# Kernel tuning notes

Measured on AMD Instinct MI355X. Metric: run time of the kernel, lower is better.

## Reference

```python
import jax, jax.numpy as jnp
import numpy as np

V_TH = 0.4
V_RESET = 0.0
REFRAC = 3.0
ALPHA = 5.0

# Heaviside spike with surrogate-gradient (fast-sigmoid) backward, matching SpikeFnSTE.
@jax.custom_vjp
def spike(x):
    return (x > 0).astype(x.dtype)

def _spike_fwd(x):
    return spike(x), x

def _spike_bwd(x, g):
    return (g * (ALPHA / (1.0 + jnp.abs(ALPHA * x)) ** 2),)

spike.defvjp(_spike_fwd, _spike_bwd)


def setup_inputs() -> dict:
    key = jax.random.key(0)
    k1, k2 = jax.random.split(key)
    B, T, F, C = 128, 1000, 2048, 10
    x_seq = jax.random.bernoulli(k1, 0.05, (B, T, F)).astype(jnp.float32)
    # kaiming_normal_ on [F, C]: fan computed over in_features
    W = jax.random.normal(k2, (F, C), dtype=jnp.float32) * np.float32(np.sqrt(2.0 / F))
    return {"x_seq": x_seq, "W": W}


def reference(x_seq, W):
    B, T, F = x_seq.shape
    C = W.shape[1]

    def step(carry, x_t):
        V, refr, counts = carry
        I_t = x_t @ W                                  # [B, C]
        active = (refr <= 0).astype(V.dtype)
        V = V + I_t * active
        s = spike(V - V_TH) * active                   # [B, C] in {0,1}
        fired = s > 0
        V = jnp.where(fired, V_RESET, V)
        counts = counts + s
        refr = jnp.where(fired, REFRAC, refr)
        refr = jnp.maximum(refr - 1.0, 0.0)
        return (V, refr, counts), None

    init = (jnp.zeros((B, C), x_seq.dtype),
            jnp.zeros((B, C), x_seq.dtype),
            jnp.zeros((B, C), x_seq.dtype))
    # scan over time: x_seq [B,T,F] -> [T,B,F]
    (_, _, spike_counts), _ = jax.lax.scan(step, init, jnp.swapaxes(x_seq, 0, 1))
    return spike_counts
```

## Files before the change

### kernel.cpp

```cpp
#include <hip/hip_runtime.h>
#include <hip/hip_bf16.h>

#define T_TOTAL 1000
#define B_TOTAL 128
#define F_TOTAL 2048
#define C_OUT   10
#define NEUR    (B_TOTAL * C_OUT)

#define KSTEPS  (F_TOTAL / 32)
#define NBFRAG  (KSTEPS * 3 * 64)

typedef __attribute__((ext_vector_type(8))) short bf16x8;
typedef __attribute__((ext_vector_type(4))) float f32x4;

__global__ __launch_bounds__(256) void snn_prep(const float* __restrict__ W,
                                                uint4* __restrict__ bfrag)
{
    const int idx = blockIdx.x * 256 + threadIdx.x;
    if (idx >= NBFRAG) return;
    const int l = idx & 63;
    const int sp = idx >> 6;
    const int p = sp % 3;
    const int s = sp / 3;
    const int g = l >> 4, r = l & 15;
    unsigned out[4] = {0u, 0u, 0u, 0u};
#pragma unroll
    for (int j = 0; j < 8; ++j) {
        const int k = s * 32 + g * 8 + j;
        const float wv = (r < C_OUT) ? W[k * C_OUT + r] : 0.f;
        __hip_bfloat16 bh = __float2bfloat16(wv);
        const float fh = __bfloat162float(bh);
        __hip_bfloat16 bm = __float2bfloat16(wv - fh);
        const float fm = __bfloat162float(bm);
        __hip_bfloat16 bl = __float2bfloat16(wv - fh - fm);
        __hip_bfloat16 sel = (p == 0) ? bh : (p == 1) ? bm : bl;
        const unsigned short bits = *reinterpret_cast<unsigned short*>(&sel);
        out[j >> 1] |= (unsigned)bits << (16 * (j & 1));
    }
    bfrag[idx] = make_uint4(out[0], out[1], out[2], out[3]);
}

__global__ __launch_bounds__(256) void snn_phase1_mfma(
    const float* __restrict__ x, const uint4* __restrict__ bfrag,
    float* __restrict__ Ibuf, int t0, int cur)
{
    const int b  = blockIdx.y;
    const int w  = threadIdx.x >> 6;
    const int l  = threadIdx.x & 63;
    const int r  = l & 15, g = l >> 4;
    const int ttbase = blockIdx.x * 64 + w * 16;

    int t_row = t0 + ttbase + r;
    if (t_row > T_TOTAL - 1) t_row = T_TOTAL - 1;
    const float* __restrict__ arow =
        x + ((size_t)b * T_TOTAL + t_row) * F_TOTAL + g * 8;

    f32x4 acc = {0.f, 0.f, 0.f, 0.f};
    const uint4* __restrict__ bp = bfrag + l;

#pragma unroll 2
    for (int s = 0; s < KSTEPS; ++s) {
        const float4 a0 = *reinterpret_cast<const float4*>(arow + s * 32);
        const float4 a1 = *reinterpret_cast<const float4*>(arow + s * 32 + 4);
        const uint4 b0 = bp[(s * 3 + 0) * 64];
        const uint4 b1 = bp[(s * 3 + 1) * 64];
        const uint4 b2 = bp[(s * 3 + 2) * 64];
        union { bf16x8 v; unsigned u[4]; } af;
        af.u[0] = __builtin_amdgcn_perm(__float_as_uint(a0.y), __float_as_uint(a0.x), 0x07060302u);
        af.u[1] = __builtin_amdgcn_perm(__float_as_uint(a0.w), __float_as_uint(a0.z), 0x07060302u);
        af.u[2] = __builtin_amdgcn_perm(__float_as_uint(a1.y), __float_as_uint(a1.x), 0x07060302u);
        af.u[3] = __builtin_amdgcn_perm(__float_as_uint(a1.w), __float_as_uint(a1.z), 0x07060302u);
        union { bf16x8 v; uint4 q; } bb0, bb1, bb2;
        bb0.q = b0; bb1.q = b1; bb2.q = b2;
        acc = __builtin_amdgcn_mfma_f32_16x16x32_bf16(af.v, bb0.v, acc, 0, 0, 0);
        acc = __builtin_amdgcn_mfma_f32_16x16x32_bf16(af.v, bb1.v, acc, 0, 0, 0);
        acc = __builtin_amdgcn_mfma_f32_16x16x32_bf16(af.v, bb2.v, acc, 0, 0, 0);
    }

    const int tt4 = ttbase + 4 * g;
    if (r < C_OUT && tt4 + 3 < cur) {
        const float4 v = make_float4(acc[0], acc[1], acc[2], acc[3]);
        *reinterpret_cast<float4*>(&Ibuf[((size_t)b * C_OUT + r) * cur + tt4]) = v;
    }
}

__device__ __forceinline__ void snn_step(float Iv, float& V, float& refr, float& cnt)
{
    const bool act = (refr <= 0.f);
    V += act ? Iv : 0.f;
    const bool fired = act && ((V - 0.4f) > 0.f);
    cnt += fired ? 1.f : 0.f;
    V    = fired ? 0.f : V;
    refr = fired ? 3.f : refr;
    refr = fmaxf(refr - 1.f, 0.f);
}

__global__ __launch_bounds__(256) void snn_phase2(
    const float* __restrict__ Ibuf, float* __restrict__ state,
    float* __restrict__ out, int t0, int Tc, int last)
{
    const int n = blockIdx.x * 256 + threadIdx.x;
    if (n >= NEUR) return;

    float V, refr, cnt;
    if (t0 == 0) { V = 0.f; refr = 0.f; cnt = 0.f; }
    else { V = state[n]; refr = state[NEUR + n]; cnt = state[2 * NEUR + n]; }

    const float* __restrict__ I = Ibuf + (size_t)n * Tc;

    int i = 0;
    for (; i + 16 <= Tc; i += 16) {
        const float4 a = *reinterpret_cast<const float4*>(I + i);
        const float4 b = *reinterpret_cast<const float4*>(I + i + 4);
        const float4 c = *reinterpret_cast<const float4*>(I + i + 8);
        const float4 d = *reinterpret_cast<const float4*>(I + i + 12);
        snn_step(a.x, V, refr, cnt); snn_step(a.y, V, refr, cnt);
        snn_step(a.z, V, refr, cnt); snn_step(a.w, V, refr, cnt);
        snn_step(b.x, V, refr, cnt); snn_step(b.y, V, refr, cnt);
        snn_step(b.z, V, refr, cnt); snn_step(b.w, V, refr, cnt);
        snn_step(c.x, V, refr, cnt); snn_step(c.y, V, refr, cnt);
        snn_step(c.z, V, refr, cnt); snn_step(c.w, V, refr, cnt);
        snn_step(d.x, V, refr, cnt); snn_step(d.y, V, refr, cnt);
        snn_step(d.z, V, refr, cnt); snn_step(d.w, V, refr, cnt);
    }
    for (; i < Tc; ++i) snn_step(I[i], V, refr, cnt);

    if (last) {
        out[n] = cnt;
    } else {
        state[n] = V; state[NEUR + n] = refr; state[2 * NEUR + n] = cnt;
    }
}

extern "C" void kernel_launch(void* const* d_in, const int* in_sizes, int n_in,
                              void* d_out, int out_size, void* d_ws, size_t ws_size,
                              hipStream_t stream)
{
    const float* x = (const float*)d_in[0];
    const float* W = (const float*)d_in[1];
    float* out = (float*)d_out;

    float* state = (float*)d_ws;
    uint4* bfrag = (uint4*)((char*)d_ws + 3 * NEUR * sizeof(float));
    float* Ibuf  = (float*)((char*)d_ws + 3 * NEUR * sizeof(float) + NBFRAG * 16);

    snn_prep<<<(NBFRAG + 255) / 256, 256, 0, stream>>>(W, bfrag);

    const size_t head = 3 * NEUR + NBFRAG * 4;
    const size_t ws_floats = ws_size / sizeof(float);
    long avail = (long)ws_floats - (long)head;
    int Tc = (avail > 0) ? (int)(avail / NEUR) : 0;
    if (Tc > T_TOTAL) Tc = T_TOTAL;
    Tc &= ~3;
    if (Tc <= 0) Tc = 4;

    for (int t0 = 0; t0 < T_TOTAL; t0 += Tc) {
        int cur = T_TOTAL - t0; if (cur > Tc) cur = Tc;
        dim3 g1((cur + 63) / 64, B_TOTAL, 1);
        snn_phase1_mfma<<<g1, 256, 0, stream>>>(x, bfrag, Ibuf, t0, cur);
        const int last = (t0 + cur >= T_TOTAL) ? 1 : 0;
        snn_phase2<<<(NEUR + 255) / 256, 256, 0, stream>>>(Ibuf, state, out, t0, cur, last);
    }
}
```

Before: 310.9 us.

## Process two time-row tiles per wave and software-pipeline the K loop

Each wave now computes two 16-row M tiles, so every loaded B fragment (the three bf16 split weight pieces) feeds two MFMAs instead of one, halving B-fragment traffic per output. The K loop is manually double-buffered so the next step's loads are issued before the current step's MFMAs. The grid shrinks to half as many blocks along time. This raises register pressure and cuts parallelism, and the kernel is likely bound by streaming the large fp32 x input anyway.

```diff
diff --git a/kernel.cpp b/kernel.cpp
--- a/kernel.cpp
+++ b/kernel.cpp
@@ -40,6 +40,36 @@
     bfrag[idx] = make_uint4(out[0], out[1], out[2], out[3]);
 }
 
+#define LOADS(S, A00, A01, A10, A11, B0, B1, B2)                              \
+    A00 = *reinterpret_cast<const float4*>(arow0 + (S) * 32);                 \
+    A01 = *reinterpret_cast<const float4*>(arow0 + (S) * 32 + 4);             \
+    A10 = *reinterpret_cast<const float4*>(arow1 + (S) * 32);                 \
+    A11 = *reinterpret_cast<const float4*>(arow1 + (S) * 32 + 4);             \
+    B0  = bp[((S) * 3 + 0) * 64];                                             \
+    B1  = bp[((S) * 3 + 1) * 64];                                             \
+    B2  = bp[((S) * 3 + 2) * 64];
+
+#define CONV(A0, A1, AF)                                                      \
+    AF.u[0] = __builtin_amdgcn_perm(__float_as_uint(A0.y), __float_as_uint(A0.x), 0x07060302u); \
+    AF.u[1] = __builtin_amdgcn_perm(__float_as_uint(A0.w), __float_as_uint(A0.z), 0x07060302u); \
+    AF.u[2] = __builtin_amdgcn_perm(__float_as_uint(A1.y), __float_as_uint(A1.x), 0x07060302u); \
+    AF.u[3] = __builtin_amdgcn_perm(__float_as_uint(A1.w), __float_as_uint(A1.z), 0x07060302u);
+
+#define STEP(A00, A01, A10, A11, B0, B1, B2)                                  \
+    {                                                                         \
+        union { bf16x8 v; unsigned u[4]; } af0, af1;                          \
+        CONV(A00, A01, af0)                                                   \
+        CONV(A10, A11, af1)                                                   \
+        union { bf16x8 v; uint4 q; } q0, q1, q2;                              \
+        q0.q = B0; q1.q = B1; q2.q = B2;                                      \
+        acc0 = __builtin_amdgcn_mfma_f32_16x16x32_bf16(af0.v, q0.v, acc0, 0, 0, 0); \
+        acc1 = __builtin_amdgcn_mfma_f32_16x16x32_bf16(af1.v, q0.v, acc1, 0, 0, 0); \
+        acc0 = __builtin_amdgcn_mfma_f32_16x16x32_bf16(af0.v, q1.v, acc0, 0, 0, 0); \
+        acc1 = __builtin_amdgcn_mfma_f32_16x16x32_bf16(af1.v, q1.v, acc1, 0, 0, 0); \
+        acc0 = __builtin_amdgcn_mfma_f32_16x16x32_bf16(af0.v, q2.v, acc0, 0, 0, 0); \
+        acc1 = __builtin_amdgcn_mfma_f32_16x16x32_bf16(af1.v, q2.v, acc1, 0, 0, 0); \
+    }
+
 __global__ __launch_bounds__(256) void snn_phase1_mfma(
     const float* __restrict__ x, const uint4* __restrict__ bfrag,
     float* __restrict__ Ibuf, int t0, int cur)
@@ -48,39 +78,48 @@
     const int w  = threadIdx.x >> 6;
     const int l  = threadIdx.x & 63;
     const int r  = l & 15, g = l >> 4;
-    const int ttbase = blockIdx.x * 64 + w * 16;
-
-    int t_row = t0 + ttbase + r;
-    if (t_row > T_TOTAL - 1) t_row = T_TOTAL - 1;
-    const float* __restrict__ arow =
-        x + ((size_t)b * T_TOTAL + t_row) * F_TOTAL + g * 8;
-
-    f32x4 acc = {0.f, 0.f, 0.f, 0.f};
+    const int ttbase = blockIdx.x * 128 + w * 32;
+
+    int t_row0 = t0 + ttbase + r;
+    int t_row1 = t_row0 + 16;
+    if (t_row0 > T_TOTAL - 1) t_row0 = T_TOTAL - 1;
+    if (t_row1 > T_TOTAL - 1) t_row1 = T_TOTAL - 1;
+    const float* __restrict__ arow0 =
+        x + ((size_t)b * T_TOTAL + t_row0) * F_TOTAL + g * 8;
+    const float* __restrict__ arow1 =
+        x + ((size_t)b * T_TOTAL + t_row1) * F_TOTAL + g * 8;
+
+    f32x4 acc0 = {0.f, 0.f, 0.f, 0.f};
+    f32x4 acc1 = {0.f, 0.f, 0.f, 0.f};
     const uint4* __restrict__ bp = bfrag + l;
 
-#pragma unroll 2
-    for (int s = 0; s < KSTEPS; ++s) {
-        const float4 a0 = *reinterpret_cast<const float4*>(arow + s * 32);
-        const float4 a1 = *reinterpret_cast<const float4*>(arow + s * 32 + 4);
-        const uint4 b0 = bp[(s * 3 + 0) * 64];
-        const uint4 b1 = bp[(s * 3 + 1) * 64];
-        const uint4 b2 = bp[(s * 3 + 2) * 64];
-        union { bf16x8 v; unsigned u[4]; } af;
-        af.u[0] = __builtin_amdgcn_perm(__float_as_uint(a0.y), __float_as_uint(a0.x), 0x07060302u);
-        af.u[1] = __builtin_amdgcn_perm(__float_as_uint(a0.w), __float_as_uint(a0.z), 0x07060302u);
-        af.u[2] = __builtin_amdgcn_perm(__float_as_uint(a1.y), __float_as_uint(a1.x), 0x07060302u);
-        af.u[3] = __builtin_amdgcn_perm(__float_as_uint(a1.w), __float_as_uint(a1.z), 0x07060302u);
-        union { bf16x8 v; uint4 q; } bb0, bb1, bb2;
-        bb0.q = b0; bb1.q = b1; bb2.q = b2;
-        acc = __builtin_amdgcn_mfma_f32_16x16x32_bf16(af.v, bb0.v, acc, 0, 0, 0);
-        acc = __builtin_amdgcn_mfma_f32_16x16x32_bf16(af.v, bb1.v, acc, 0, 0, 0);
-        acc = __builtin_amdgcn_mfma_f32_16x16x32_bf16(af.v, bb2.v, acc, 0, 0, 0);
-    }
-
-    const int tt4 = ttbase + 4 * g;
-    if (r < C_OUT && tt4 + 3 < cur) {
-        const float4 v = make_float4(acc[0], acc[1], acc[2], acc[3]);
-        *reinterpret_cast<float4*>(&Ibuf[((size_t)b * C_OUT + r) * cur + tt4]) = v;
+    float4 cA00, cA01, cA10, cA11; uint4 cB0, cB1, cB2;
+    float4 nA00, nA01, nA10, nA11; uint4 nB0, nB1, nB2;
+
+    LOADS(0, cA00, cA01, cA10, cA11, cB0, cB1, cB2)
+
+#pragma unroll 1
+    for (int s = 0; s < KSTEPS - 2; s += 2) {
+        LOADS(s + 1, nA00, nA01, nA10, nA11, nB0, nB1, nB2)
+        STEP(cA00, cA01, cA10, cA11, cB0, cB1, cB2)
+        LOADS(s + 2, cA00, cA01, cA10, cA11, cB0, cB1, cB2)
+        STEP(nA00, nA01, nA10, nA11, nB0, nB1, nB2)
+    }
+    LOADS(KSTEPS - 1, nA00, nA01, nA10, nA11, nB0, nB1, nB2)
+    STEP(cA00, cA01, cA10, cA11, cB0, cB1, cB2)
+    STEP(nA00, nA01, nA10, nA11, nB0, nB1, nB2)
+
+    const int tt4_0 = ttbase + 4 * g;
+    const int tt4_1 = tt4_0 + 16;
+    if (r < C_OUT) {
+        if (tt4_0 + 3 < cur) {
+            const float4 v = make_float4(acc0[0], acc0[1], acc0[2], acc0[3]);
+            *reinterpret_cast<float4*>(&Ibuf[((size_t)b * C_OUT + r) * cur + tt4_0]) = v;
+        }
+        if (tt4_1 + 3 < cur) {
+            const float4 v = make_float4(acc1[0], acc1[1], acc1[2], acc1[3]);
+            *reinterpret_cast<float4*>(&Ibuf[((size_t)b * C_OUT + r) * cur + tt4_1]) = v;
+        }
     }
 }
 
@@ -156,7 +195,7 @@
 
     for (int t0 = 0; t0 < T_TOTAL; t0 += Tc) {
         int cur = T_TOTAL - t0; if (cur > Tc) cur = Tc;
-        dim3 g1((cur + 63) / 64, B_TOTAL, 1);
+        dim3 g1((cur + 127) / 128, B_TOTAL, 1);
         snn_phase1_mfma<<<g1, 256, 0, stream>>>(x, bfrag, Ibuf, t0, cur);
         const int last = (t0 + cur >= T_TOTAL) ? 1 : 0;
         snn_phase2<<<(NEUR + 255) / 256, 256, 0, stream>>>(Ibuf, state, out, t0, cur, last);
```

Measured after the change: 286.2 us, median of 2. -8.0%, faster.

## Give each wave four M-tiles and double-buffer A/B loads in the MFMA loop

Applied to the files above, without the earlier changes.

Each wavefront now computes four 16-row time tiles instead of one, so every B-fragment load from the precomputed split-bf16 weights is reused across four MFMA chains. The K loop is software-pipelined with two register buffer sets, so the loads for the next step are issued before the MFMAs of the current step. The grid shrinks by four in the time dimension. This costs many more VGPRs for the prefetched x rows and accumulators, which may lower occupancy on a kernel that is mostly memory bound.

```diff
diff --git a/kernel.cpp b/kernel.cpp
--- a/kernel.cpp
+++ b/kernel.cpp
@@ -12,6 +12,7 @@
 
 typedef __attribute__((ext_vector_type(8))) short bf16x8;
 typedef __attribute__((ext_vector_type(4))) float f32x4;
+typedef __attribute__((ext_vector_type(4))) unsigned u32x4;
 
 __global__ __launch_bounds__(256) void snn_prep(const float* __restrict__ W,
                                                 uint4* __restrict__ bfrag)
@@ -48,39 +49,82 @@
     const int w  = threadIdx.x >> 6;
     const int l  = threadIdx.x & 63;
     const int r  = l & 15, g = l >> 4;
-    const int ttbase = blockIdx.x * 64 + w * 16;
-
-    int t_row = t0 + ttbase + r;
-    if (t_row > T_TOTAL - 1) t_row = T_TOTAL - 1;
-    const float* __restrict__ arow =
-        x + ((size_t)b * T_TOTAL + t_row) * F_TOTAL + g * 8;
-
-    f32x4 acc = {0.f, 0.f, 0.f, 0.f};
+    const int ttbase = blockIdx.x * 256 + w * 64;
+
+    const float* __restrict__ arow[4];
+#pragma unroll
+    for (int i = 0; i < 4; ++i) {
+        int t_row = t0 + ttbase + 16 * i + r;
+        if (t_row > T_TOTAL - 1) t_row = T_TOTAL - 1;
+        arow[i] = x + ((size_t)b * T_TOTAL + t_row) * F_TOTAL + g * 8;
+    }
+
+    f32x4 acc[4];
+#pragma unroll
+    for (int i = 0; i < 4; ++i) acc[i] = (f32x4){0.f, 0.f, 0.f, 0.f};
+
     const uint4* __restrict__ bp = bfrag + l;
 
-#pragma unroll 2
-    for (int s = 0; s < KSTEPS; ++s) {
-        const float4 a0 = *reinterpret_cast<const float4*>(arow + s * 32);
-        const float4 a1 = *reinterpret_cast<const float4*>(arow + s * 32 + 4);
-        const uint4 b0 = bp[(s * 3 + 0) * 64];
-        const uint4 b1 = bp[(s * 3 + 1) * 64];
-        const uint4 b2 = bp[(s * 3 + 2) * 64];
-        union { bf16x8 v; unsigned u[4]; } af;
-        af.u[0] = __builtin_amdgcn_perm(__float_as_uint(a0.y), __float_as_uint(a0.x), 0x07060302u);
-        af.u[1] = __builtin_amdgcn_perm(__float_as_uint(a0.w), __float_as_uint(a0.z), 0x07060302u);
-        af.u[2] = __builtin_amdgcn_perm(__float_as_uint(a1.y), __float_as_uint(a1.x), 0x07060302u);
-        af.u[3] = __builtin_amdgcn_perm(__float_as_uint(a1.w), __float_as_uint(a1.z), 0x07060302u);
-        union { bf16x8 v; uint4 q; } bb0, bb1, bb2;
-        bb0.q = b0; bb1.q = b1; bb2.q = b2;
-        acc = __builtin_amdgcn_mfma_f32_16x16x32_bf16(af.v, bb0.v, acc, 0, 0, 0);
-        acc = __builtin_amdgcn_mfma_f32_16x16x32_bf16(af.v, bb1.v, acc, 0, 0, 0);
-        acc = __builtin_amdgcn_mfma_f32_16x16x32_bf16(af.v, bb2.v, acc, 0, 0, 0);
-    }
-
-    const int tt4 = ttbase + 4 * g;
-    if (r < C_OUT && tt4 + 3 < cur) {
-        const float4 v = make_float4(acc[0], acc[1], acc[2], acc[3]);
-        *reinterpret_cast<float4*>(&Ibuf[((size_t)b * C_OUT + r) * cur + tt4]) = v;
+    u32x4 cA[8], nA[8];
+    uint4 cB[3], nB[3];
+
+#define LOADS(S, A, Bf)                                                       \
+    {                                                                         \
+        _Pragma("unroll")                                                     \
+        for (int i = 0; i < 4; ++i) {                                         \
+            A[2 * i]     = *reinterpret_cast<const u32x4*>(arow[i] + (S) * 32);     \
+            A[2 * i + 1] = *reinterpret_cast<const u32x4*>(arow[i] + (S) * 32 + 4); \
+        }                                                                     \
+        Bf[0] = bp[((S) * 3 + 0) * 64];                                       \
+        Bf[1] = bp[((S) * 3 + 1) * 64];                                       \
+        Bf[2] = bp[((S) * 3 + 2) * 64];                                       \
+    }
+
+#define STEP(A, Bf)                                                           \
+    {                                                                         \
+        union { bf16x8 v; unsigned u[4]; } af[4];                             \
+        _Pragma("unroll")                                                     \
+        for (int i = 0; i < 4; ++i) {                                         \
+            af[i].u[0] = __builtin_amdgcn_perm(A[2*i][1],   A[2*i][0],   0x07060302u); \
+            af[i].u[1] = __builtin_amdgcn_perm(A[2*i][3],   A[2*i][2],   0x07060302u); \
+            af[i].u[2] = __builtin_amdgcn_perm(A[2*i+1][1], A[2*i+1][0], 0x07060302u); \
+            af[i].u[3] = __builtin_amdgcn_perm(A[2*i+1][3], A[2*i+1][2], 0x07060302u); \
+        }                                                                     \
+        union { bf16x8 v; uint4 q; } q0, q1, q2;                              \
+        q0.q = Bf[0]; q1.q = Bf[1]; q2.q = Bf[2];                             \
+        _Pragma("unroll")                                                     \
+        for (int i = 0; i < 4; ++i) {                                         \
+            acc[i] = __builtin_amdgcn_mfma_f32_16x16x32_bf16(af[i].v, q0.v, acc[i], 0, 0, 0); \
+            acc[i] = __builtin_amdgcn_mfma_f32_16x16x32_bf16(af[i].v, q1.v, acc[i], 0, 0, 0); \
+            acc[i] = __builtin_amdgcn_mfma_f32_16x16x32_bf16(af[i].v, q2.v, acc[i], 0, 0, 0); \
+        }                                                                     \
+    }
+
+    LOADS(0, cA, cB)
+
+#pragma unroll 1
+    for (int s = 0; s < KSTEPS - 2; s += 2) {
+        LOADS(s + 1, nA, nB)
+        STEP(cA, cB)
+        LOADS(s + 2, cA, cB)
+        STEP(nA, nB)
+    }
+    LOADS(KSTEPS - 1, nA, nB)
+    STEP(cA, cB)
+    STEP(nA, nB)
+
+#undef LOADS
+#undef STEP
+
+    if (r < C_OUT) {
+#pragma unroll
+        for (int i = 0; i < 4; ++i) {
+            const int tt4 = ttbase + 16 * i + 4 * g;
+            if (tt4 + 3 < cur) {
+                const float4 v = make_float4(acc[i][0], acc[i][1], acc[i][2], acc[i][3]);
+                *reinterpret_cast<float4*>(&Ibuf[((size_t)b * C_OUT + r) * cur + tt4]) = v;
+            }
+        }
     }
 }
 
@@ -156,7 +200,7 @@
 
     for (int t0 = 0; t0 < T_TOTAL; t0 += Tc) {
         int cur = T_TOTAL - t0; if (cur > Tc) cur = Tc;
-        dim3 g1((cur + 63) / 64, B_TOTAL, 1);
+        dim3 g1((cur + 255) / 256, B_TOTAL, 1);
         snn_phase1_mfma<<<g1, 256, 0, stream>>>(x, bfrag, Ibuf, t0, cur);
         const int last = (t0 + cur >= T_TOTAL) ? 1 : 0;
         snn_phase2<<<(NEUR + 255) / 256, 256, 0, stream>>>(Ibuf, state, out, t0, cur, last);
```

Measured after the change: 291.3 us. 6.3% less time.
